# Kernel tuning notes

Measured on AMD Instinct MI355X. Metric: run time of the kernel, lower is better.

Reference implementation:

```python
import jax, jax.numpy as jnp
from jax import lax
import numpy as np

B, T, D, Z, ENC, DEC = 512, 128, 128, 64, 512, 512


def lstm_layer(x, Wx, Wh, b):
    """Keras-style LSTM, return_sequences=True, zero initial state.
    x: [B,T,Din], Wx: [Din,4U], Wh: [U,4U], b: [4U]. Gate order i,f,c,o."""
    Bx = x.shape[0]
    U = Wh.shape[0]
    # precompute input projections for all timesteps: [T,B,4U]
    xw = jnp.swapaxes(jnp.einsum('btd,dg->btg', x, Wx) + b, 0, 1)

    def step(carry, xt):
        h, c = carry
        g = xt + h @ Wh                      # [B,4U]
        i, f, gg, o = jnp.split(g, 4, axis=-1)
        i = jax.nn.sigmoid(i)
        f = jax.nn.sigmoid(f)
        gg = jnp.tanh(gg)
        o = jax.nn.sigmoid(o)
        c = f * c + i * gg
        h = o * jnp.tanh(c)
        return (h, c), h

    init = (jnp.zeros((Bx, U), x.dtype), jnp.zeros((Bx, U), x.dtype))
    _, hs = lax.scan(step, init, xw)
    return jnp.swapaxes(hs, 0, 1)            # [B,T,U]


def setup_inputs() -> dict:
    key = jax.random.key(0)
    ks = jax.random.split(key, 20)
    s = 0.05  # weight scale for numerical stability
    return {
        'x': jax.random.normal(ks[0], (B, T, D), jnp.float32),
        'epsilon': jax.random.normal(ks[1], (B, T, Z), jnp.float32),
        'e0_Wx': jax.random.normal(ks[2], (D, 4 * ENC), jnp.float32) * s,
        'e0_Wh': jax.random.normal(ks[3], (ENC, 4 * ENC), jnp.float32) * s,
        'e0_b': jnp.zeros((4 * ENC,), jnp.float32),
        'e1_Wx': jax.random.normal(ks[4], (ENC, 4 * ENC), jnp.float32) * s,
        'e1_Wh': jax.random.normal(ks[5], (ENC, 4 * ENC), jnp.float32) * s,
        'e1_b': jnp.zeros((4 * ENC,), jnp.float32),
        'd0_Wx': jax.random.normal(ks[6], (Z, 4 * DEC), jnp.float32) * s,
        'd0_Wh': jax.random.normal(ks[7], (DEC, 4 * DEC), jnp.float32) * s,
        'd0_b': jnp.zeros((4 * DEC,), jnp.float32),
        'd1_Wx': jax.random.normal(ks[8], (DEC, 4 * DEC), jnp.float32) * s,
        'd1_Wh': jax.random.normal(ks[9], (DEC, 4 * DEC), jnp.float32) * s,
        'd1_b': jnp.zeros((4 * DEC,), jnp.float32),
        'Wm': jax.random.normal(ks[10], (ENC, Z), jnp.float32) * s,
        'bm': jnp.zeros((Z,), jnp.float32),
        'Wv': jax.random.normal(ks[11], (ENC, Z), jnp.float32) * s,
        'bv': jnp.zeros((Z,), jnp.float32),
        'Wo': jax.random.normal(ks[12], (DEC, D), jnp.float32) * s,
        'bo': jnp.zeros((D,), jnp.float32),
    }


def reference(x, epsilon, e0_Wx, e0_Wh, e0_b, e1_Wx, e1_Wh, e1_b,
              d0_Wx, d0_Wh, d0_b, d1_Wx, d1_Wh, d1_b,
              Wm, bm, Wv, bv, Wo, bo):
    # encoder: 2 stacked LSTMs (eval mode -> no dropout)
    h = lstm_layer(x, e0_Wx, e0_Wh, e0_b)
    h = lstm_layer(h, e1_Wx, e1_Wh, e1_b)
    z_mean = h @ Wm + bm                     # [B,T,Z]
    z_log_var = h @ Wv + bv                  # [B,T,Z]
    # reparameterize
    z = z_mean + jnp.exp(0.5 * z_log_var) * epsilon
    # decoder: 2 stacked LSTMs + output Dense
    g = lstm_layer(z, d0_Wx, d0_Wh, d0_b)
    g = lstm_layer(g, d1_Wx, d1_Wh, d1_b)
    reconstructed = g @ Wo + bo              # [B,T,D]
    return (reconstructed, jnp.exp(z_log_var), z_mean, z_log_var, z)
```

## Files before the change

kernel.cpp:

```cpp
#include <hip/hip_runtime.h>
#include <hip/hip_bf16.h>


#define B_  512
#define T_  128
#define D_  128
#define Z_  64
#define U_  512
#define G4_ 2048

typedef __attribute__((ext_vector_type(8))) short short8;
typedef __attribute__((ext_vector_type(4))) float f32x4;
typedef unsigned long long ull;

__device__ __forceinline__ float tanhf_(float x){ return 2.0f / (1.0f + __expf(-2.0f * x)) - 1.0f; }


__global__ void convert_transpose(const float* __restrict__ src, __hip_bfloat16* __restrict__ dst) {
    int i = blockIdx.x * 256 + threadIdx.x;
    if (i >= B_ * T_ * D_) return;
    int t = i >> 16;
    int rem = i & 65535;
    int b = rem >> 7, d = rem & 127;
    dst[i] = __float2bfloat16(src[((size_t)b * T_ + t) * D_ + d]);
}

__global__ void conv_weight(const float* __restrict__ src, __hip_bfloat16* __restrict__ dst,
                            int K, int Nrows, int Nsrc, int ldd, int koff, int perm) {
    int idx = blockIdx.x * 256 + threadIdx.x;
    if (idx >= K * Nrows) return;
    int n = idx / K, k = idx - n * K;
    int pc = perm ? ((n & 3) * 512 + (n >> 2)) : n;
    dst[(size_t)n * ldd + koff + k] = __float2bfloat16(src[(size_t)k * Nsrc + pc]);
}

__global__ void conv_bias(const float* __restrict__ src, float* __restrict__ dst) {
    int n = blockIdx.x * 256 + threadIdx.x;
    if (n < G4_) dst[n] = src[(n & 3) * 512 + (n >> 2)];
}

template <int DIN>
__global__ __launch_bounds__(256, 1) void lstm_layer_persist(
    __hip_bfloat16* __restrict__ hs,
    const __hip_bfloat16* __restrict__ xin,
    const __hip_bfloat16* __restrict__ WT,
    const float* __restrict__ bias,
    unsigned* __restrict__ ctrl) {
    constexpr bool WX_LDS = (DIN <= 128);
    constexpr int LDW = U_ + DIN;
    constexpr int SX = DIN * 2;
    __shared__ __hip_bfloat16 WhL[64 * 512];
    __shared__ __hip_bfloat16 hL[64 * 512];
    __shared__ __hip_bfloat16 WxL[WX_LDS ? 64 * DIN : 64];
    __shared__ __hip_bfloat16 hstage[64 * 16];
    __shared__ unsigned sj;

    const int tid = threadIdx.x;
    const int w = tid >> 6, l = tid & 63, lr = l & 15, lq = l >> 4;
    const int wm = (w >> 1) * 32, wn = (w & 1) * 32;
    const int gate = l & 3;

    unsigned xcc;
    asm volatile("s_getreg_b32 %0, hwreg(HW_REG_XCC_ID)" : "=s"(xcc));
    const int g = (int)(xcc & 7);
    if (tid == 0)
        sj = __hip_atomic_fetch_add(ctrl + g, 1u, __ATOMIC_RELAXED, __HIP_MEMORY_SCOPE_AGENT);
    __syncthreads();
    const int j = (int)(sj & 31);
    const int m0 = g * 64, n0 = j * 64;
    unsigned* gflags = ctrl + 64 + g * (32 * 16);
    unsigned* myflag = gflags + j * 16;

    for (int idx = tid; idx < 64 * 64; idx += 256) {
        int row = idx >> 6, ch = idx & 63;
        short8 v = *(const short8*)(WT + (size_t)(n0 + row) * LDW + ch * 8);
        int byte = row * 1024 + ((ch * 16) ^ ((row & 7) << 4));
        *(short8*)((char*)WhL + byte) = v;
    }
    if constexpr (WX_LDS) {
        constexpr int CHX = DIN / 8;
        for (int idx = tid; idx < 64 * CHX; idx += 256) {
            int row = idx / CHX, ch = idx - row * CHX;
            short8 v = *(const short8*)(WT + (size_t)(n0 + row) * LDW + U_ + ch * 8);
            int byte = row * SX + ((ch * 16) ^ ((row & 7) << 4));
            *(short8*)((char*)WxL + byte) = v;
        }
    }

    const float b0v = bias[n0 + wn + lr];
    const float b1v = bias[n0 + wn + 16 + lr];

    float c_reg[2][2][4];
#pragma unroll
    for (int i = 0; i < 2; i++)
#pragma unroll
        for (int jj = 0; jj < 2; jj++)
#pragma unroll
            for (int r = 0; r < 4; r++) c_reg[i][jj][r] = 0.0f;

    const int rowA0 = m0 + wm + lr, rowA1 = rowA0 + 16;
    const int rB0 = wn + lr, rB1 = wn + 16 + lr;
    const int sw = (lr & 7) << 4;
    const char* WhB0 = (const char*)WhL + rB0 * 1024;
    const char* WhB1 = (const char*)WhL + rB1 * 1024;
    const char* hA0  = (const char*)hL + (wm + lr) * 1024;
    const char* hA1  = (const char*)hL + (wm + 16 + lr) * 1024;

    __syncthreads();

    for (int t = 0; t < T_; ++t) {
        f32x4 acc[2][2];
#pragma unroll
        for (int i = 0; i < 2; i++)
#pragma unroll
            for (int r = 0; r < 4; r++) { acc[i][0][r] = b0v; acc[i][1][r] = b1v; }

        {
            const __hip_bfloat16* X0 = xin + ((size_t)t * B_ + rowA0) * DIN + lq * 8;
            const __hip_bfloat16* X1 = xin + ((size_t)t * B_ + rowA1) * DIN + lq * 8;
#pragma unroll
            for (int k0 = 0; k0 < DIN; k0 += 32) {
                short8 a0 = *(const short8*)(X0 + k0);
                short8 a1 = *(const short8*)(X1 + k0);
                short8 bb0, bb1;
                if constexpr (WX_LDS) {
                    int off = (k0 + lq * 8) * 2;
                    bb0 = *(const short8*)((const char*)WxL + rB0 * SX + (off ^ sw));
                    bb1 = *(const short8*)((const char*)WxL + rB1 * SX + (off ^ sw));
                } else {
                    bb0 = *(const short8*)(WT + (size_t)(n0 + rB0) * LDW + U_ + k0 + lq * 8);
                    bb1 = *(const short8*)(WT + (size_t)(n0 + rB1) * LDW + U_ + k0 + lq * 8);
                }
                acc[0][0] = __builtin_amdgcn_mfma_f32_16x16x32_bf16(a0, bb0, acc[0][0], 0, 0, 0);
                acc[0][1] = __builtin_amdgcn_mfma_f32_16x16x32_bf16(a0, bb1, acc[0][1], 0, 0, 0);
                acc[1][0] = __builtin_amdgcn_mfma_f32_16x16x32_bf16(a1, bb0, acc[1][0], 0, 0, 0);
                acc[1][1] = __builtin_amdgcn_mfma_f32_16x16x32_bf16(a1, bb1, acc[1][1], 0, 0, 0);
            }
        }

        if (t > 0) {
            if (tid < 32) {
                const unsigned* f = gflags + tid * 16;
                while (__hip_atomic_load(f, __ATOMIC_RELAXED, __HIP_MEMORY_SCOPE_AGENT) < (unsigned)t)
                    __builtin_amdgcn_s_sleep(1);
            }
            __syncthreads();

            {
                const short8* hsrc = (const short8*)(hs + ((size_t)(t - 1) * B_ + m0) * U_);
                short8 buf[16];
#pragma unroll
                for (int c = 0; c < 16; ++c) buf[c] = hsrc[c * 256 + tid];
#pragma unroll
                for (int c = 0; c < 16; ++c) {
                    int ci = c * 256 + tid;
                    int row = ci >> 6, ch = ci & 63;
                    int byte = row * 1024 + ((ch * 16) ^ ((row & 7) << 4));
                    *(short8*)((char*)hL + byte) = buf[c];
                }
            }
            __syncthreads();

#pragma unroll 8
            for (int k0 = 0; k0 < U_; k0 += 32) {
                int off = (k0 + lq * 8) * 2;
                short8 a0 = *(const short8*)(hA0 + (off ^ sw));
                short8 a1 = *(const short8*)(hA1 + (off ^ sw));
                short8 bb0 = *(const short8*)(WhB0 + (off ^ sw));
                short8 bb1 = *(const short8*)(WhB1 + (off ^ sw));
                acc[0][0] = __builtin_amdgcn_mfma_f32_16x16x32_bf16(a0, bb0, acc[0][0], 0, 0, 0);
                acc[0][1] = __builtin_amdgcn_mfma_f32_16x16x32_bf16(a0, bb1, acc[0][1], 0, 0, 0);
                acc[1][0] = __builtin_amdgcn_mfma_f32_16x16x32_bf16(a1, bb0, acc[1][0], 0, 0, 0);
                acc[1][1] = __builtin_amdgcn_mfma_f32_16x16x32_bf16(a1, bb1, acc[1][1], 0, 0, 0);
            }
        }

#pragma unroll
        for (int i = 0; i < 2; i++)
#pragma unroll
            for (int jj = 0; jj < 2; jj++) {
#pragma unroll
                for (int r = 0; r < 4; r++) {
                    float v = acc[i][jj][r];
                    float e = __expf((gate == 2) ? -2.0f * v : -v);
                    float s = 1.0f / (1.0f + e);
                    acc[i][jj][r] = (gate == 2) ? 2.0f * s - 1.0f : s;
                }
#pragma unroll
                for (int r = 0; r < 4; r++) {
                    float nv = acc[i][jj][r];
                    float f1 = __shfl_xor(nv, 1);
                    float f2 = __shfl_xor(nv, 2);
                    float f3 = __shfl_xor(nv, 3);
                    if (gate == 0) {
                        float cn = f1 * c_reg[i][jj][r] + nv * f2;
                        c_reg[i][jj][r] = cn;
                        float hv = f3 * tanhf_(cn);
                        int lrow = wm + i * 16 + lq * 4 + r;
                        int lu = (wn + jj * 16 + lr) >> 2;
                        hstage[lrow * 16 + lu] = __float2bfloat16(hv);
                    }
                }
            }

        __syncthreads();

        if (tid < 128) {
            int lrow = tid >> 1, half = tid & 1;
            short8 X = *(const short8*)(hstage + lrow * 16 + half * 8);
            *(short8*)(hs + ((size_t)t * B_ + m0 + lrow) * U_ + j * 16 + half * 8) = X;
        }

        if (t < T_ - 1) {
            __syncthreads();
            if (tid == 0)
                __hip_atomic_store(myflag, (unsigned)(t + 1), __ATOMIC_RELAXED, __HIP_MEMORY_SCOPE_AGENT);
        }
    }
}

__global__ __launch_bounds__(256) void gemm_bias(
    const __hip_bfloat16* __restrict__ A, const __hip_bfloat16* __restrict__ WT,
    const float* __restrict__ bias, float* __restrict__ out, int K, int N) {
    const int m0 = blockIdx.x * 128, n0 = blockIdx.y * 64;
    const int tid = threadIdx.x, w = tid >> 6, l = tid & 63, lr = l & 15, lq = l >> 4;
    const int wm = w * 32;

    f32x4 acc[2][4];
#pragma unroll
    for (int jj = 0; jj < 4; jj++) {
        float bv = bias[n0 + jj * 16 + lr];
#pragma unroll
        for (int i = 0; i < 2; i++)
#pragma unroll
            for (int r = 0; r < 4; r++) acc[i][jj][r] = bv;
    }
    for (int k0 = 0; k0 < K; k0 += 32) {
        short8 a[2], b[4];
#pragma unroll
        for (int i = 0; i < 2; i++)
            a[i] = *(const short8*)(A + (size_t)(m0 + wm + i * 16 + lr) * K + k0 + lq * 8);
#pragma unroll
        for (int jj = 0; jj < 4; jj++)
            b[jj] = *(const short8*)(WT + (size_t)(n0 + jj * 16 + lr) * K + k0 + lq * 8);
#pragma unroll
        for (int i = 0; i < 2; i++)
#pragma unroll
            for (int jj = 0; jj < 4; jj++)
                acc[i][jj] = __builtin_amdgcn_mfma_f32_16x16x32_bf16(a[i], b[jj], acc[i][jj], 0, 0, 0);
    }
#pragma unroll
    for (int i = 0; i < 2; i++)
#pragma unroll
        for (int jj = 0; jj < 4; jj++)
#pragma unroll
            for (int r = 0; r < 4; r++) {
                int ra = m0 + wm + i * 16 + lq * 4 + r;
                int rh = (ra & 511) * T_ + (ra >> 9);
                out[(size_t)rh * N + n0 + jj * 16 + lr] = acc[i][jj][r];
            }
}

__global__ void reparam(const float* __restrict__ zm, const float* __restrict__ zlv,
                        const float* __restrict__ eps, float* __restrict__ z,
                        float* __restrict__ ezlv, __hip_bfloat16* __restrict__ zb, int n) {
    int i = blockIdx.x * 256 + threadIdx.x;
    if (i >= n) return;
    float m = zm[i], lv = zlv[i];
    float zi = m + expf(0.5f * lv) * eps[i];
    z[i] = zi;
    ezlv[i] = expf(lv);
    int b = i >> 13;
    int rem = i & 8191;
    int t = rem >> 6, zc = rem & 63;
    zb[(((size_t)t << 9) + b) * Z_ + zc] = __float2bfloat16(zi);
}


extern "C" void kernel_launch(void* const* d_in, const int* in_sizes, int n_in,
                              void* d_out, int out_size, void* d_ws, size_t ws_size,
                              hipStream_t stream) {
    const float* x    = (const float*)d_in[0];
    const float* eps  = (const float*)d_in[1];
    const float* e0Wx = (const float*)d_in[2];
    const float* e0Wh = (const float*)d_in[3];
    const float* e0b  = (const float*)d_in[4];
    const float* e1Wx = (const float*)d_in[5];
    const float* e1Wh = (const float*)d_in[6];
    const float* e1b  = (const float*)d_in[7];
    const float* d0Wx = (const float*)d_in[8];
    const float* d0Wh = (const float*)d_in[9];
    const float* d0b  = (const float*)d_in[10];
    const float* d1Wx = (const float*)d_in[11];
    const float* d1Wh = (const float*)d_in[12];
    const float* d1b  = (const float*)d_in[13];
    const float* Wm   = (const float*)d_in[14];
    const float* bm   = (const float*)d_in[15];
    const float* Wv   = (const float*)d_in[16];
    const float* bv   = (const float*)d_in[17];
    const float* Wo   = (const float*)d_in[18];
    const float* bo   = (const float*)d_in[19];
    float* out = (float*)d_out;

    char* ws = (char*)d_ws;
    size_t off = 0;
    auto alloc = [&](size_t bytes) -> char* {
        off = (off + 255) & ~(size_t)255;
        char* p = ws + off;
        off += bytes;
        return p;
    };
    __hip_bfloat16* hsA  = (__hip_bfloat16*)alloc((size_t)B_ * T_ * U_ * 2);
    __hip_bfloat16* hsB  = (__hip_bfloat16*)alloc((size_t)B_ * T_ * U_ * 2);
    __hip_bfloat16* xb   = (__hip_bfloat16*)alloc((size_t)B_ * T_ * D_ * 2);
    __hip_bfloat16* zb   = (__hip_bfloat16*)alloc((size_t)B_ * T_ * Z_ * 2);
    __hip_bfloat16* WTe0 = (__hip_bfloat16*)alloc((size_t)G4_ * (U_ + D_) * 2);
    __hip_bfloat16* WTe1 = (__hip_bfloat16*)alloc((size_t)G4_ * (U_ + U_) * 2);
    __hip_bfloat16* WTd0 = (__hip_bfloat16*)alloc((size_t)G4_ * (U_ + Z_) * 2);
    __hip_bfloat16* WTd1 = (__hip_bfloat16*)alloc((size_t)G4_ * (U_ + U_) * 2);
    __hip_bfloat16* WmT  = (__hip_bfloat16*)alloc((size_t)Z_ * U_ * 2);
    __hip_bfloat16* WvT  = (__hip_bfloat16*)alloc((size_t)Z_ * U_ * 2);
    __hip_bfloat16* WoT  = (__hip_bfloat16*)alloc((size_t)D_ * U_ * 2);
    float* be0 = (float*)alloc(G4_ * 4);
    float* be1 = (float*)alloc(G4_ * 4);
    float* bd0 = (float*)alloc(G4_ * 4);
    float* bd1 = (float*)alloc(G4_ * 4);
    const int CTRLW = 64 + 4096;
    unsigned* ctrl = (unsigned*)alloc((size_t)4 * CTRLW * sizeof(unsigned));

    hipMemsetAsync(ctrl, 0, (size_t)4 * CTRLW * sizeof(unsigned), stream);

    convert_transpose<<<(B_ * T_ * D_ + 255) / 256, 256, 0, stream>>>(x, xb);

    auto cw = [&](const float* src, __hip_bfloat16* dst, int K, int Nrows, int Nsrc, int ldd, int koff, int perm) {
        conv_weight<<<(K * Nrows + 255) / 256, 256, 0, stream>>>(src, dst, K, Nrows, Nsrc, ldd, koff, perm);
    };
    cw(e0Wh, WTe0, U_, G4_, G4_, U_ + D_, 0, 1);
    cw(e0Wx, WTe0, D_, G4_, G4_, U_ + D_, U_, 1);
    cw(e1Wh, WTe1, U_, G4_, G4_, U_ + U_, 0, 1);
    cw(e1Wx, WTe1, U_, G4_, G4_, U_ + U_, U_, 1);
    cw(d0Wh, WTd0, U_, G4_, G4_, U_ + Z_, 0, 1);
    cw(d0Wx, WTd0, Z_, G4_, G4_, U_ + Z_, U_, 1);
    cw(d1Wh, WTd1, U_, G4_, G4_, U_ + U_, 0, 1);
    cw(d1Wx, WTd1, U_, G4_, G4_, U_ + U_, U_, 1);
    cw(Wm, WmT, U_, Z_, Z_, U_, 0, 0);
    cw(Wv, WvT, U_, Z_, Z_, U_, 0, 0);
    cw(Wo, WoT, U_, D_, D_, U_, 0, 0);
    conv_bias<<<G4_ / 256, 256, 0, stream>>>(e0b, be0);
    conv_bias<<<G4_ / 256, 256, 0, stream>>>(e1b, be1);
    conv_bias<<<G4_ / 256, 256, 0, stream>>>(d0b, bd0);
    conv_bias<<<G4_ / 256, 256, 0, stream>>>(d1b, bd1);

    lstm_layer_persist<D_><<<256, 256, 0, stream>>>(hsA, xb, WTe0, be0, ctrl + 0 * CTRLW);
    lstm_layer_persist<U_><<<256, 256, 0, stream>>>(hsB, hsA, WTe1, be1, ctrl + 1 * CTRLW);

    const size_t oRecon = 0;
    const size_t oE   = (size_t)B_ * T_ * D_;
    const size_t oZm  = oE + (size_t)B_ * T_ * Z_;
    const size_t oZlv = oZm + (size_t)B_ * T_ * Z_;
    const size_t oZ   = oZlv + (size_t)B_ * T_ * Z_;

    gemm_bias<<<dim3(B_ * T_ / 128, Z_ / 64), 256, 0, stream>>>(hsB, WmT, bm, out + oZm, U_, Z_);
    gemm_bias<<<dim3(B_ * T_ / 128, Z_ / 64), 256, 0, stream>>>(hsB, WvT, bv, out + oZlv, U_, Z_);
    reparam<<<(B_ * T_ * Z_ + 255) / 256, 256, 0, stream>>>(out + oZm, out + oZlv, eps,
                                                            out + oZ, out + oE, zb, B_ * T_ * Z_);

    lstm_layer_persist<Z_><<<256, 256, 0, stream>>>(hsA, zb, WTd0, bd0, ctrl + 2 * CTRLW);
    lstm_layer_persist<U_><<<256, 256, 0, stream>>>(hsB, hsA, WTd1, bd1, ctrl + 3 * CTRLW);

    gemm_bias<<<dim3(B_ * T_ / 128, D_ / 64), 256, 0, stream>>>(hsB, WoT, bo, out + oRecon, U_, D_);
}
```

Baseline: 4.052 ms.

## Pipeline per-producer flag waits with h loads and write h directly from registers

```diff
diff --git a/kernel.cpp b/kernel.cpp
--- a/kernel.cpp
+++ b/kernel.cpp
@@ -52,13 +52,13 @@
     __shared__ __hip_bfloat16 WhL[64 * 512];
     __shared__ __hip_bfloat16 hL[64 * 512];
     __shared__ __hip_bfloat16 WxL[WX_LDS ? 64 * DIN : 64];
-    __shared__ __hip_bfloat16 hstage[64 * 16];
     __shared__ unsigned sj;
 
     const int tid = threadIdx.x;
     const int w = tid >> 6, l = tid & 63, lr = l & 15, lq = l >> 4;
     const int wm = (w >> 1) * 32, wn = (w & 1) * 32;
     const int gate = l & 3;
+    const int pbase = w * 8;
 
     unsigned xcc;
     asm volatile("s_getreg_b32 %0, hwreg(HW_REG_XCC_ID)" : "=s"(xcc));
@@ -101,10 +101,12 @@
     const int rowA0 = m0 + wm + lr, rowA1 = rowA0 + 16;
     const int rB0 = wn + lr, rB1 = wn + 16 + lr;
     const int sw = (lr & 7) << 4;
+    const int swl = (l & 7) << 4;
     const char* WhB0 = (const char*)WhL + rB0 * 1024;
     const char* WhB1 = (const char*)WhL + rB1 * 1024;
     const char* hA0  = (const char*)hL + (wm + lr) * 1024;
     const char* hA1  = (const char*)hL + (wm + 16 + lr) * 1024;
+    char* hrow = (char*)hL + l * 1024;
 
     __syncthreads();
 
@@ -139,25 +141,30 @@
         }
 
         if (t > 0) {
-            if (tid < 32) {
-                const unsigned* f = gflags + tid * 16;
-                while (__hip_atomic_load(f, __ATOMIC_RELAXED, __HIP_MEMORY_SCOPE_AGENT) < (unsigned)t)
-                    __builtin_amdgcn_s_sleep(1);
-            }
-            __syncthreads();
-
-            {
-                const short8* hsrc = (const short8*)(hs + ((size_t)(t - 1) * B_ + m0) * U_);
-                short8 buf[16];
-#pragma unroll
-                for (int c = 0; c < 16; ++c) buf[c] = hsrc[c * 256 + tid];
-#pragma unroll
-                for (int c = 0; c < 16; ++c) {
-                    int ci = c * 256 + tid;
-                    int row = ci >> 6, ch = ci & 63;
-                    int byte = row * 1024 + ((ch * 16) ^ ((row & 7) << 4));
-                    *(short8*)((char*)hL + byte) = buf[c];
+            unsigned fv = 0xFFFFFFFFu;
+            if (l < 8)
+                fv = __hip_atomic_load(gflags + (pbase + l) * 16, __ATOMIC_RELAXED, __HIP_MEMORY_SCOPE_AGENT);
+            ull rdy = __ballot(fv >= (unsigned)t);
+
+            short8 buf0[8], buf1[8];
+            const __hip_bfloat16* hrowsrc = hs + ((size_t)(t - 1) * B_ + m0 + l) * U_;
+#pragma unroll
+            for (int pp = 0; pp < 8; ++pp) {
+                int p = pbase + pp;
+                if (!((rdy >> pp) & 1)) {
+                    const unsigned* f = gflags + p * 16;
+                    while (__hip_atomic_load(f, __ATOMIC_RELAXED, __HIP_MEMORY_SCOPE_AGENT) < (unsigned)t)
+                        __builtin_amdgcn_s_sleep(1);
                 }
+                const short8* src = (const short8*)(hrowsrc + p * 16);
+                buf0[pp] = src[0];
+                buf1[pp] = src[1];
+            }
+#pragma unroll
+            for (int pp = 0; pp < 8; ++pp) {
+                int p = pbase + pp;
+                *(short8*)(hrow + ((p * 32) ^ swl)) = buf0[pp];
+                *(short8*)(hrow + ((p * 32 + 16) ^ swl)) = buf1[pp];
             }
             __syncthreads();
 
@@ -192,30 +199,31 @@
                     float f1 = __shfl_xor(nv, 1);
                     float f2 = __shfl_xor(nv, 2);
                     float f3 = __shfl_xor(nv, 3);
+                    unsigned hb = 0;
                     if (gate == 0) {
                         float cn = f1 * c_reg[i][jj][r] + nv * f2;
                         c_reg[i][jj][r] = cn;
                         float hv = f3 * tanhf_(cn);
-                        int lrow = wm + i * 16 + lq * 4 + r;
-                        int lu = (wn + jj * 16 + lr) >> 2;
-                        hstage[lrow * 16 + lu] = __float2bfloat16(hv);
+                        __hip_bfloat16 hbf = __float2bfloat16(hv);
+                        unsigned short us;
+                        __builtin_memcpy(&us, &hbf, 2);
+                        hb = us;
+                    }
+                    unsigned px  = __shfl_xor(hb, 4);
+                    unsigned w2w = hb | (px << 16);
+                    unsigned hi  = __shfl_xor(w2w, 8);
+                    if ((l & 15) == 0) {
+                        ull v64 = (ull)w2w | ((ull)hi << 32);
+                        int row = m0 + wm + i * 16 + lq * 4 + r;
+                        int ub = (n0 + wn + jj * 16) >> 2;
+                        *(ull*)(hs + ((size_t)t * B_ + row) * U_ + ub) = v64;
                     }
                 }
             }
 
         __syncthreads();
-
-        if (tid < 128) {
-            int lrow = tid >> 1, half = tid & 1;
-            short8 X = *(const short8*)(hstage + lrow * 16 + half * 8);
-            *(short8*)(hs + ((size_t)t * B_ + m0 + lrow) * U_ + j * 16 + half * 8) = X;
-        }
-
-        if (t < T_ - 1) {
-            __syncthreads();
-            if (tid == 0)
-                __hip_atomic_store(myflag, (unsigned)(t + 1), __ATOMIC_RELAXED, __HIP_MEMORY_SCOPE_AGENT);
-        }
+        if (t < T_ - 1 && tid == 0)
+            __hip_atomic_store(myflag, (unsigned)(t + 1), __ATOMIC_RELAXED, __HIP_MEMORY_SCOPE_AGENT);
     }
 }
 
```

Result: slower. 5.097 ms (+25.8%).
